# Kernel tuning notes

Measured on AMD Instinct MI355X. Metric: run time of the kernel, lower is better.

## Reference

```python
import jax, jax.numpy as jnp
import numpy as np

C = 256        # n_channels
CQK = 32       # n_query_key_channels (C // 8)
B = 16
HT, WT = 16, 16   # template feature map
HS, WS = 32, 32   # search-region feature map
K = 9             # 3x3 deformable kernel taps


def _conv1x1(x, w, b):
    # x [B,C,H,W], w [Co,Ci], b [Co]
    return jnp.einsum('bchw,oc->bohw', x, w) + b[None, :, None, None]


def _conv3x3(x, w, b):
    y = jax.lax.conv_general_dilated(x, w, (1, 1), 'SAME',
                                     dimension_numbers=('NCHW', 'OIHW', 'NCHW'))
    return y + b[None, :, None, None]


def _spatial_self_attn(x, qw, qb, kw, kb, vw, vb, weight=1.0):
    Bn, Cn, H, W = x.shape
    N = H * W
    q = _conv1x1(x, qw, qb).reshape(Bn, -1, N)   # [B,Cqk,N]
    k = _conv1x1(x, kw, kb).reshape(Bn, -1, N)
    v = _conv1x1(x, vw, vb).reshape(Bn, Cn, N)
    att = jnp.einsum('bcn,bcm->bnm', q, k)       # q^T k -> [B,N,N], no scaling (faithful)
    att = jax.nn.softmax(att, axis=0)            # softmax over BATCH dim, as in source
    out = weight * jnp.einsum('bcn,bnm->bcm', v, att)
    return out.reshape(x.shape)


def _channel_self_attn(x, weight=1.0):
    Bn, Cn, H, W = x.shape
    f = x.reshape(Bn, Cn, H * W)
    att = jnp.einsum('bcn,bdn->bcd', f, f)       # [B,C,C]
    att = jax.nn.softmax(att, axis=1)            # softmax over dim=1 (faithful)
    out = weight * jnp.einsum('bcd,bdn->bcn', att, f)
    return out.reshape(x.shape)


def _cross_attn(src, dst, weight=1.0):
    Bn, Cn = src.shape[:2]
    s = src.reshape(Bn, Cn, -1)
    d = dst.reshape(Bn, Cn, -1)
    att = jnp.einsum('bcn,bdn->bcd', s, s)       # CxC map from src only
    att = jax.nn.softmax(att, axis=1)
    out = weight * jnp.einsum('bcd,bdn->bcn', att, d)
    return out.reshape(dst.shape)


def _bilinear(img, y, x):
    # img [B,C,H,W]; y,x [B,K,H,W] float sampling coords -> [B,C,K,H,W], zeros outside
    Bn, Cn, H, W = img.shape
    y0 = jnp.floor(y)
    x0 = jnp.floor(x)
    wy1 = y - y0
    wx1 = x - x0

    def g(yi, xi):
        valid = ((yi >= 0) & (yi <= H - 1) & (xi >= 0) & (xi <= W - 1)).astype(img.dtype)
        yc = jnp.clip(yi, 0, H - 1).astype(jnp.int32)
        xc = jnp.clip(xi, 0, W - 1).astype(jnp.int32)
        bidx = jnp.arange(Bn)[:, None, None, None]
        v = img[bidx, :, yc, xc]                 # [B,K,H,W,C]
        return jnp.moveaxis(v, -1, 1) * valid[:, None]

    return (g(y0, x0) * ((1 - wy1) * (1 - wx1))[:, None]
            + g(y0, x0 + 1) * ((1 - wy1) * wx1)[:, None]
            + g(y0 + 1, x0) * (wy1 * (1 - wx1))[:, None]
            + g(y0 + 1, x0 + 1) * (wy1 * wx1)[:, None])


def _mod_deform_conv3x3(x, off_w, off_b, w, b):
    # mmcv ModulatedDeformConvPack: conv_offset -> chunk(o1,o2,mask); offset=cat(o1,o2); mask=sigmoid
    Bn, Cn, H, W = x.shape
    oo = _conv3x3(x, off_w, off_b)               # [B, 27, H, W]
    o1, o2, m = jnp.split(oo, 3, axis=1)
    offset = jnp.concatenate([o1, o2], axis=1)   # [B, 18, H, W]
    mask = jax.nn.sigmoid(m)                     # [B, 9, H, W]
    off_y = offset[:, 0::2]                      # channel 2k  -> y offset of tap k
    off_x = offset[:, 1::2]                      # channel 2k+1-> x offset of tap k
    ki, kj = jnp.meshgrid(jnp.arange(3), jnp.arange(3), indexing='ij')
    ki = ki.reshape(K).astype(jnp.float32)
    kj = kj.reshape(K).astype(jnp.float32)
    # stride 1, pad 1, dilation 1
    y = jnp.arange(H, dtype=jnp.float32)[None, None, :, None] - 1.0 + ki[None, :, None, None] + off_y
    xx = jnp.arange(W, dtype=jnp.float32)[None, None, None, :] - 1.0 + kj[None, :, None, None] + off_x
    sampled = _bilinear(x, y, xx) * mask[:, None]   # [B,C,K,H,W]
    out = jnp.einsum('bckhw,ock->bohw', sampled, w.reshape(w.shape[0], Cn, K))
    return out + b[None, :, None, None]


def _forward(template_features, sr_features,
             tq_w, tq_b, tk_w, tk_b, tv_w, tv_b,
             sq_w, sq_b, sk_w, sk_b, sv_w, sv_b,
             t_off_w, t_off_b, t_dcn_w, t_dcn_b,
             s_off_w, s_off_b, s_dcn_w, s_dcn_b):
    t, s = template_features, sr_features
    t_self = _spatial_self_attn(t, tq_w, tq_b, tk_w, tk_b, tv_w, tv_b) + _channel_self_attn(t)
    t_cross = _cross_attn(s, t)
    s_self = _spatial_self_attn(s, sq_w, sq_b, sk_w, sk_b, sv_w, sv_b) + _channel_self_attn(s)
    s_cross = _cross_attn(t, s)
    at = t + t_self + t_cross
    asr = s + s_self + s_cross
    out_t = _mod_deform_conv3x3(at, t_off_w, t_off_b, t_dcn_w, t_dcn_b)
    out_s = _mod_deform_conv3x3(asr, s_off_w, s_off_b, s_dcn_w, s_dcn_b)
    return (out_t, out_s)


def setup_inputs() -> dict:
    key = jax.random.key(0)
    ks = jax.random.split(key, 16)

    def rn(k, shape, s=1.0):
        return s * jax.random.normal(k, shape, dtype=jnp.float32)

    w1 = 1.0 / np.sqrt(C)          # 1x1 conv fan-in scale
    wd = 1.0 / np.sqrt(C * K)      # 3x3 conv fan-in scale
    inp = {
        'template_features': rn(ks[0], (B, C, HT, WT)),
        'sr_features': rn(ks[1], (B, C, HS, WS)),
        'tq_w': rn(ks[2], (CQK, C), w1), 'tq_b': jnp.zeros((CQK,), jnp.float32),
        'tk_w': rn(ks[3], (CQK, C), w1), 'tk_b': jnp.zeros((CQK,), jnp.float32),
        'tv_w': rn(ks[4], (C, C), w1), 'tv_b': jnp.zeros((C,), jnp.float32),
        'sq_w': rn(ks[5], (CQK, C), w1), 'sq_b': jnp.zeros((CQK,), jnp.float32),
        'sk_w': rn(ks[6], (CQK, C), w1), 'sk_b': jnp.zeros((CQK,), jnp.float32),
        'sv_w': rn(ks[7], (C, C), w1), 'sv_b': jnp.zeros((C,), jnp.float32),
        't_off_w': rn(ks[8], (3 * K, C, 3, 3), 0.01), 't_off_b': jnp.zeros((3 * K,), jnp.float32),
        't_dcn_w': rn(ks[9], (C, C, 3, 3), wd), 't_dcn_b': jnp.zeros((C,), jnp.float32),
        's_off_w': rn(ks[10], (3 * K, C, 3, 3), 0.01), 's_off_b': jnp.zeros((3 * K,), jnp.float32),
        's_dcn_w': rn(ks[11], (C, C, 3, 3), wd), 's_dcn_b': jnp.zeros((C,), jnp.float32),
    }
    return inp


def reference(template_features, sr_features,
              tq_w, tq_b, tk_w, tk_b, tv_w, tv_b,
              sq_w, sq_b, sk_w, sk_b, sv_w, sv_b,
              t_off_w, t_off_b, t_dcn_w, t_dcn_b,
              s_off_w, s_off_b, s_dcn_w, s_dcn_b):
    return _forward(template_features, sr_features,
                    tq_w, tq_b, tk_w, tk_b, tv_w, tv_b,
                    sq_w, sq_b, sk_w, sk_b, sv_w, sv_b,
                    t_off_w, t_off_b, t_dcn_w, t_dcn_b,
                    s_off_w, s_off_b, s_dcn_w, s_dcn_b)
```

## Files before the change

kernel.cpp:

```cpp
#include <hip/hip_runtime.h>
#include <hip/hip_bf16.h>

typedef __hip_bfloat16 bf16;
typedef __attribute__((ext_vector_type(8))) short short8;
typedef __attribute__((ext_vector_type(4))) short short4v;
typedef __attribute__((ext_vector_type(4))) float f32x4;

__device__ __forceinline__ short f2b(float v)
{
    union { bf16 b; short s; } u;
    u.b = __float2bfloat16(v);
    return u.s;
}
__device__ __forceinline__ float b2f(short s)
{
    union { short s; bf16 b; } u;
    u.s = s;
    return __bfloat162float(u.b);
}
__device__ __forceinline__ void splt(float v, short& hi, short& lo)
{
    hi = f2b(v);
    lo = f2b(v - b2f(hi));
}
__device__ __forceinline__ int bsw(int row, int g)
{
    return row * 40 + (((g + (row >> 3)) & 3) << 3);
}

__global__ void detect_k(const unsigned short* __restrict__ p, int* __restrict__ flag)
{
    __shared__ int cnt;
    if (threadIdx.x == 0) cnt = 0;
    __syncthreads();
    int bad = 0;
    for (int i = threadIdx.x; i < 4096; i += 256) {
        unsigned short u = p[2 * i];
        int e = (u >> 7) & 0xFF;
        if (e != 0 && (e < 100 || e > 140)) bad++;
    }
    atomicAdd(&cnt, bad);
    __syncthreads();
    if (threadIdx.x == 0) *flag = (cnt > 1024) ? 1 : 0;
}

#define NSEG 24
struct IArgs {
    const void* src[NSEG];
    float* dst[NSEG];
    long start[NSEG + 1];
};

__global__ void ingest_all_k(IArgs a, const int* __restrict__ flag)
{
    long i = (long)blockIdx.x * 256 + threadIdx.x;
    if (i >= a.start[NSEG]) return;
    int s = 0;
#pragma unroll
    for (int j = 1; j < NSEG; j++) s += (i >= a.start[j]) ? 1 : 0;
    long idx = i - a.start[s];
    float v;
    if (*flag) v = ((const float*)a.src[s])[idx];
    else       v = __bfloat162float(((const bf16*)a.src[s])[idx]);
    a.dst[s][idx] = v;
}

__global__ void fill_k(float* __restrict__ C, const float* __restrict__ bias,
                       long MN, int Nn, long total)
{
    long i = (long)blockIdx.x * 256 + threadIdx.x;
    if (i >= total) return;
    float v = 0.f;
    if (bias) {
        long r = i % MN;
        v = bias[(int)(r / Nn)];
    }
    C[i] = v;
}

__global__ void fillo_k(float* __restrict__ C1, const float* __restrict__ b1,
                        int N1, long tot1,
                        float* __restrict__ C2, const float* __restrict__ b2,
                        int N2, long tot2)
{
    long i = (long)blockIdx.x * 256 + threadIdx.x;
    if (i < tot1) {
        long r = i % ((long)27 * N1);
        C1[i] = b1[(int)(r / N1)];
    } else {
        i -= tot1;
        if (i < tot2) {
            long r = i % ((long)27 * N2);
            C2[i] = b2[(int)(r / N2)];
        }
    }
}

__global__ void tr2_k(const float* __restrict__ X1, float* __restrict__ T1, int N1,
                      const float* __restrict__ X2, float* __restrict__ T2, int N2)
{
    __shared__ float t[32][33];
    int bx = blockIdx.x;
    const float* X; float* T; int N, n0;
    int nb1 = N1 / 32;
    if (bx < nb1) { X = X1; T = T1; N = N1; n0 = bx * 32; }
    else          { X = X2; T = T2; N = N2; n0 = (bx - nb1) * 32; }
    int b = blockIdx.z, c0 = blockIdx.y * 32;
    const float* Xb = X + (long)b * 256 * N;
    float* Tb = T + (long)b * 256 * N;
    int tx = threadIdx.x, ty = threadIdx.y;
#pragma unroll
    for (int i = 0; i < 4; i++)
        t[ty + 8 * i][tx] = Xb[(long)(c0 + ty + 8 * i) * N + n0 + tx];
    __syncthreads();
#pragma unroll
    for (int i = 0; i < 4; i++)
        Tb[(long)(n0 + ty + 8 * i) * 256 + c0 + tx] = t[tx][ty + 8 * i];
}

template <bool TRA, int BMODE, bool ACCUM, bool BIAS, int PREC, int KSPLIT>
__launch_bounds__(256)
__global__ void mgemm(const float* __restrict__ A, int lda, int ksA, long sA,
                      const void* __restrict__ Bsrc, int ldb, long sB,
                      float* __restrict__ C, int ldc, long sC,
                      const float* __restrict__ bias,
                      int M, int N, int K, int H, int wsh)
{
    __shared__ short As[PREC * 2560];
    __shared__ short Bs[PREC * 2560];

    const int bz = blockIdx.z;
    const float* Ab = A + (long)bz * sA;
    float* Cb = C + (long)bz * sC;
    const int mt = blockIdx.y / KSPLIT, ch = blockIdx.y % KSPLIT;
    const int m0 = mt * 64, n0 = blockIdx.x * 64;
    const int kchunk = K / KSPLIT;
    const int kbeg = ch * kchunk, kend = kbeg + kchunk;
    const int tid = threadIdx.x;

    f32x4 acc[2][2];
#pragma unroll
    for (int i = 0; i < 2; i++)
#pragma unroll
        for (int j = 0; j < 2; j++) acc[i][j] = (f32x4){0.f, 0.f, 0.f, 0.f};

    const int lane = tid & 63, wv = tid >> 6;
    const int moff = (wv & 1) * 32, noff = (wv >> 1) * 32;
    const int lr = lane & 15, lq = lane >> 4;
    const int mm = tid >> 2, kk0 = (tid & 3) * 8;
    const int nn = tid & 63, kg = tid >> 6;

    for (int k0 = kbeg; k0 < kend; k0 += 32) {
        {
            float vv[8];
            if (m0 + mm < M) {
                if (!TRA) {
                    if (ksA == 1) {
                        const float4* s4 = (const float4*)(Ab + (long)(m0 + mm) * lda + k0 + kk0);
                        float4 v0 = s4[0], v1 = s4[1];
                        vv[0] = v0.x; vv[1] = v0.y; vv[2] = v0.z; vv[3] = v0.w;
                        vv[4] = v1.x; vv[5] = v1.y; vv[6] = v1.z; vv[7] = v1.w;
                    } else {
                        const float* s = Ab + (long)(m0 + mm) * lda + (long)(k0 + kk0) * ksA;
#pragma unroll
                        for (int j = 0; j < 8; j++) vv[j] = s[(long)j * ksA];
                    }
                } else {
#pragma unroll
                    for (int j = 0; j < 8; j++)
                        vv[j] = Ab[(long)(k0 + kk0 + j) * lda + m0 + mm];
                }
            } else {
#pragma unroll
                for (int j = 0; j < 8; j++) vv[j] = 0.f;
            }
            short8 hi, lo;
#pragma unroll
            for (int j = 0; j < 8; j++) { short h, l; splt(vv[j], h, l); hi[j] = h; lo[j] = l; }
            *(short8*)&As[mm * 40 + kk0] = hi;
            if (PREC == 2) *(short8*)&As[2560 + mm * 40 + kk0] = lo;
        }

        if (BMODE == 1) {
            const float4* s4 = (const float4*)((const float*)Bsrc + (long)bz * sB +
                                               (long)(n0 + mm) * ldb + k0 + kk0);
            float4 v0 = s4[0], v1 = s4[1];
            float vv[8] = {v0.x, v0.y, v0.z, v0.w, v1.x, v1.y, v1.z, v1.w};
            short8 hi, lo;
#pragma unroll
            for (int j = 0; j < 8; j++) { short h, l; splt(vv[j], h, l); hi[j] = h; lo[j] = l; }
            int o = bsw(mm, tid & 3);
            *(short8*)&Bs[o] = hi;
            if (PREC == 2) *(short8*)&Bs[2560 + o] = lo;
        } else {
            float vv[8];
            if (BMODE == 0) {
#pragma unroll
                for (int j = 0; j < 8; j++)
                    vv[j] = ((const float*)Bsrc)[(long)bz * sB + (long)(k0 + kg * 8 + j) * ldb + n0 + nn];
            } else {
                int W = 1 << wsh;
                int n = n0 + nn;
                int hbase = n >> wsh, wbase = n & (W - 1);
#pragma unroll
                for (int j = 0; j < 8; j++) {
                    int kc = k0 + kg * 8 + j;
                    int c = kc / 9, tap = kc - 9 * c;
                    int h = hbase + tap / 3 - 1, w = wbase + tap % 3 - 1;
                    vv[j] = (h >= 0 && h < H && w >= 0 && w < W)
                          ? ((const float*)Bsrc)[(long)bz * sB + (long)c * ldb + (h << wsh) + w]
                          : 0.f;
                }
            }
            short8 hi, lo;
#pragma unroll
            for (int j = 0; j < 8; j++) { short h, l; splt(vv[j], h, l); hi[j] = h; lo[j] = l; }
            int o = bsw(nn, kg);
            *(short8*)&Bs[o] = hi;
            if (PREC == 2) *(short8*)&Bs[2560 + o] = lo;
        }
        __syncthreads();

        int rb0 = noff + lr, rb1 = noff + 16 + lr;
        short8 a0h = *(short8*)&As[(moff + lr) * 40 + lq * 8];
        short8 a1h = *(short8*)&As[(moff + 16 + lr) * 40 + lq * 8];
        short8 b0h = *(short8*)&Bs[bsw(rb0, lq)];
        short8 b1h = *(short8*)&Bs[bsw(rb1, lq)];
        acc[0][0] = __builtin_amdgcn_mfma_f32_16x16x32_bf16(a0h, b0h, acc[0][0], 0, 0, 0);
        acc[0][1] = __builtin_amdgcn_mfma_f32_16x16x32_bf16(a0h, b1h, acc[0][1], 0, 0, 0);
        acc[1][0] = __builtin_amdgcn_mfma_f32_16x16x32_bf16(a1h, b0h, acc[1][0], 0, 0, 0);
        acc[1][1] = __builtin_amdgcn_mfma_f32_16x16x32_bf16(a1h, b1h, acc[1][1], 0, 0, 0);
        if (PREC == 2) {
            short8 a0l = *(short8*)&As[2560 + (moff + lr) * 40 + lq * 8];
            short8 a1l = *(short8*)&As[2560 + (moff + 16 + lr) * 40 + lq * 8];
            short8 b0l = *(short8*)&Bs[2560 + bsw(rb0, lq)];
            short8 b1l = *(short8*)&Bs[2560 + bsw(rb1, lq)];
            acc[0][0] = __builtin_amdgcn_mfma_f32_16x16x32_bf16(a0h, b0l, acc[0][0], 0, 0, 0);
            acc[0][1] = __builtin_amdgcn_mfma_f32_16x16x32_bf16(a0h, b1l, acc[0][1], 0, 0, 0);
            acc[1][0] = __builtin_amdgcn_mfma_f32_16x16x32_bf16(a1h, b0l, acc[1][0], 0, 0, 0);
            acc[1][1] = __builtin_amdgcn_mfma_f32_16x16x32_bf16(a1h, b1l, acc[1][1], 0, 0, 0);
            acc[0][0] = __builtin_amdgcn_mfma_f32_16x16x32_bf16(a0l, b0h, acc[0][0], 0, 0, 0);
            acc[0][1] = __builtin_amdgcn_mfma_f32_16x16x32_bf16(a0l, b1h, acc[0][1], 0, 0, 0);
            acc[1][0] = __builtin_amdgcn_mfma_f32_16x16x32_bf16(a1l, b0h, acc[1][0], 0, 0, 0);
            acc[1][1] = __builtin_amdgcn_mfma_f32_16x16x32_bf16(a1l, b1h, acc[1][1], 0, 0, 0);
        }
        __syncthreads();
    }

#pragma unroll
    for (int mi = 0; mi < 2; mi++)
#pragma unroll
        for (int ni = 0; ni < 2; ni++) {
            int col = n0 + noff + ni * 16 + lr;
#pragma unroll
            for (int r = 0; r < 4; r++) {
                int row = m0 + moff + mi * 16 + lq * 4 + r;
                if (row < M) {
                    long o = (long)row * ldc + col;
                    float v = acc[mi][ni][r];
                    if (KSPLIT > 1) {
                        atomicAdd(&Cb[o], v);
                    } else {
                        if (BIAS) v += bias[row];
                        if (ACCUM) v += Cb[o];
                        Cb[o] = v;
                    }
                }
            }
        }
}

__global__ void dcnw2_k(const float* __restrict__ OOt, float4* __restrict__ Twt,
                        int4* __restrict__ Tat,
                        const float* __restrict__ OOs, float4* __restrict__ Tws,
                        int4* __restrict__ Tas)
{
    long idx = (long)blockIdx.x * 256 + threadIdx.x;
    const long n1 = 16L * 9 * 256;
    const long n2 = 16L * 9 * 1024;
    const float* OO; float4* Tw; int4* Ta; int N, H, W;
    if (idx < n1) { OO = OOt; Tw = Twt; Ta = Tat; N = 256; H = 16; W = 16; }
    else {
        idx -= n1;
        if (idx >= n2) return;
        OO = OOs; Tw = Tws; Ta = Tas; N = 1024; H = 32; W = 32;
    }
    int b = (int)(idx / (9 * N));
    int r = (int)(idx % (9 * N));
    int tap = r / N, p = r % N;
    int h = p / W, w = p % W;
    const float* oob = OO + (long)b * 27 * N;
    float oy = oob[(2 * tap) * N + p];
    float ox = oob[(2 * tap + 1) * N + p];
    float mz = oob[(18 + tap) * N + p];
    float mask = 1.f / (1.f + expf(-mz));
    float y = (float)(h - 1 + tap / 3) + oy;
    float x = (float)(w - 1 + tap % 3) + ox;
    float y0 = floorf(y), x0 = floorf(x);
    float wy = y - y0, wx = x - x0;
    float ys[2] = {y0, y0 + 1.f};
    float xs[2] = {x0, x0 + 1.f};
    float wys[2] = {1.f - wy, wy};
    float wxs[2] = {1.f - wx, wx};
    float wv[4]; int av[4];
#pragma unroll
    for (int iy = 0; iy < 2; iy++)
#pragma unroll
        for (int ix = 0; ix < 2; ix++) {
            float yy = ys[iy], xx = xs[ix];
            bool valid = (yy >= 0.f) && (yy <= (float)(H - 1)) &&
                         (xx >= 0.f) && (xx <= (float)(W - 1));
            wv[iy * 2 + ix] = valid ? wys[iy] * wxs[ix] * mask : 0.f;
            int yc = (int)fminf(fmaxf(yy, 0.f), (float)(H - 1));
            int xc = (int)fminf(fmaxf(xx, 0.f), (float)(W - 1));
            av[iy * 2 + ix] = yc * W + xc;
        }
    long o = (long)(b * 9 + tap) * N + p;
    Tw[o] = (float4){wv[0], wv[1], wv[2], wv[3]};
    Ta[o] = (int4){av[0], av[1], av[2], av[3]};
}

__global__ void wre5_k(const float* __restrict__ Wt, short* __restrict__ Wht,
                       const float* __restrict__ Ws, short* __restrict__ Whs)
{
    long idx = (long)blockIdx.x * 256 + threadIdx.x;
    const long half = 2304L * 256;
    const float* W; short* Wh;
    if (idx < half) { W = Wt; Wh = Wht; }
    else            { W = Ws; Wh = Whs; idx -= half; }
    int o = (int)(idx / 2304);
    int k = (int)(idx % 2304);
    int tap = k >> 8, c = k & 255;
    Wh[(long)o * 2304 + tap * 256 + c] = f2b(W[((long)o * 256 + c) * 9 + tap]);
}

__global__ void samp2_k(const float4* __restrict__ Twt, const int4* __restrict__ Tat,
                        const float* __restrict__ XTt, short* __restrict__ Sit,
                        const float4* __restrict__ Tws, const int4* __restrict__ Tas,
                        const float* __restrict__ XTs, short* __restrict__ Sis)
{
    int bx = blockIdx.x;
    const float4* Tw; const int4* Ta; const float* XT; short* Si;
    int N, NRND, nblk;
    if (bx < 4) { Tw = Twt; Ta = Tat; XT = XTt; Si = Sit; N = 256;  NRND = 256;  nblk = bx; }
    else        { Tw = Tws; Ta = Tas; XT = XTs; Si = Sis; N = 1024; NRND = 1024; nblk = bx - 4; }

    int tid = threadIdx.x;
    int g = tid >> 2, cc2 = tid & 3;
    int tap = blockIdx.y, b = blockIdx.z;
    int n = nblk * 64 + g;
    long ti = ((long)(b * 9 + tap)) * N + n;
    float4 w4 = Tw[ti];
    int4 a4 = Ta[ti];
    const float* Xb = XT + (long)b * 256 * N;
    const float4* r0 = (const float4*)(Xb + (long)a4.x * 256);
    const float4* r1 = (const float4*)(Xb + (long)a4.y * 256);
    const float4* r2 = (const float4*)(Xb + (long)a4.z * 256);
    const float4* r3 = (const float4*)(Xb + (long)a4.w * 256);
    long so = ((long)b * NRND + n) * 2304 + tap * 256;
    short4v out[16];
#pragma unroll
    for (int q = 0; q < 16; q++) {
        int i = q * 4 + cc2;
        float4 p = r0[i], qv = r1[i], s = r2[i], t = r3[i];
        out[q][0] = f2b(w4.x * p.x + w4.y * qv.x + w4.z * s.x + w4.w * t.x);
        out[q][1] = f2b(w4.x * p.y + w4.y * qv.y + w4.z * s.y + w4.w * t.y);
        out[q][2] = f2b(w4.x * p.z + w4.y * qv.z + w4.z * s.z + w4.w * t.z);
        out[q][3] = f2b(w4.x * p.w + w4.y * qv.w + w4.z * s.w + w4.w * t.w);
    }
#pragma unroll
    for (int q = 0; q < 16; q++)
        *(short4v*)&Si[so + q * 16 + cc2 * 4] = out[q];
}

__launch_bounds__(256, 4)
__global__ void dcn9_k(const short* __restrict__ Wh_s, const short* __restrict__ Si_s,
                       const short* __restrict__ Wh_t, const short* __restrict__ Si_t,
                       const float* __restrict__ bias_s, const float* __restrict__ bias_t,
                       float* __restrict__ Cs, float* __restrict__ Ct)
{
    __shared__ float red[8192];

    int bid = blockIdx.x;
    const short* Wh; const short* Si; const float* bias; float* Cb;
    int N, mt, nt;
    if (bid < 1024) {
        int bz = bid >> 6, t = bid & 63;
        mt = t >> 4; nt = t & 15;
        Wh = Wh_s; Si = Si_s + (long)bz * 1024 * 2304;
        bias = bias_s; Cb = Cs + (long)bz * 256 * 1024; N = 1024;
    } else {
        int r = bid - 1024;
        int bz = r >> 4, t = r & 15;
        mt = t >> 2; nt = t & 3;
        Wh = Wh_t; Si = Si_t + (long)bz * 256 * 2304;
        bias = bias_t; Cb = Ct + (long)bz * 256 * 256; N = 256;
    }
    const int m0 = mt * 64, n0 = nt * 64;

    const int tid = threadIdx.x;
    const int lane = tid & 63, wv = tid >> 6;
    const int lr = lane & 15, lq = lane >> 4;

    int aoff[4], boff[4];
#pragma unroll
    for (int mi = 0; mi < 4; mi++)
        aoff[mi] = (m0 + mi * 16 + lr) * 2304 + lq * 8;
#pragma unroll
    for (int ni = 0; ni < 4; ni++)
        boff[ni] = (n0 + ni * 16 + lr) * 2304 + lq * 8;

    f32x4 acc[4][4];
#pragma unroll
    for (int i = 0; i < 4; i++)
#pragma unroll
        for (int j = 0; j < 4; j++) acc[i][j] = (f32x4){0.f, 0.f, 0.f, 0.f};

    const int kbeg = wv * 18;
#pragma unroll 2
    for (int kt = kbeg; kt < kbeg + 18; kt++) {
        int koff = (kt >> 3) * 256 + (kt & 7) * 32;
        short8 ah[4], bh[4];
#pragma unroll
        for (int ni = 0; ni < 4; ni++)
            bh[ni] = *(const short8*)&Si[boff[ni] + koff];
#pragma unroll
        for (int mi = 0; mi < 4; mi++)
            ah[mi] = *(const short8*)&Wh[aoff[mi] + koff];
#pragma unroll
        for (int mi = 0; mi < 4; mi++)
#pragma unroll
            for (int ni = 0; ni < 4; ni++)
                acc[mi][ni] = __builtin_amdgcn_mfma_f32_16x16x32_bf16(ah[mi], bh[ni], acc[mi][ni], 0, 0, 0);
    }

    if (wv == 1 || wv == 3) {
        float* rp = &red[(wv == 1 ? 0 : 4096) + lane];
#pragma unroll
        for (int mi = 0; mi < 4; mi++)
#pragma unroll
            for (int ni = 0; ni < 4; ni++)
#pragma unroll
                for (int r2 = 0; r2 < 4; r2++)
                    rp[(mi * 16 + ni * 4 + r2) << 6] = acc[mi][ni][r2];
    }
    __syncthreads();
    if (wv == 0) {
        const float* rp = &red[lane];
#pragma unroll
        for (int mi = 0; mi < 4; mi++)
#pragma unroll
            for (int ni = 0; ni < 4; ni++)
#pragma unroll
                for (int r2 = 0; r2 < 4; r2++)
                    acc[mi][ni][r2] += rp[(mi * 16 + ni * 4 + r2) << 6];
    } else if (wv == 2) {
        float* rp = &red[4096 + lane];
#pragma unroll
        for (int mi = 0; mi < 4; mi++)
#pragma unroll
            for (int ni = 0; ni < 4; ni++)
#pragma unroll
                for (int r2 = 0; r2 < 4; r2++) {
                    int o = (mi * 16 + ni * 4 + r2) << 6;
                    float v = acc[mi][ni][r2] + rp[o];
                    rp[o] = v;
                }
    }
    __syncthreads();
    if (wv == 0) {
        const float* rp = &red[4096 + lane];
#pragma unroll
        for (int mi = 0; mi < 4; mi++)
#pragma unroll
            for (int ni = 0; ni < 4; ni++) {
                int col = n0 + ni * 16 + lr;
#pragma unroll
                for (int r2 = 0; r2 < 4; r2++) {
                    int row = m0 + mi * 16 + lq * 4 + r2;
                    float v = acc[mi][ni][r2] + rp[(mi * 16 + ni * 4 + r2) << 6];
                    Cb[(long)row * N + col] = v + bias[row];
                }
            }
    }
}

__global__ void softmax_b_k(float* __restrict__ att, long NN)
{
    long idx = (long)blockIdx.x * 256 + threadIdx.x;
    if (idx >= NN) return;
    float r[16];
    float mx = -1e30f;
#pragma unroll
    for (int b = 0; b < 16; b++) {
        r[b] = att[(long)b * NN + idx];
        mx = fmaxf(mx, r[b]);
    }
    float s = 0.f;
#pragma unroll
    for (int b = 0; b < 16; b++) { r[b] = expf(r[b] - mx); s += r[b]; }
    float inv = 1.f / s;
#pragma unroll
    for (int b = 0; b < 16; b++) att[(long)b * NN + idx] = r[b] * inv;
}

__global__ void gram_sm_k(const float* __restrict__ gt, const float* __restrict__ gs,
                          float* __restrict__ Mo)
{
    int b = blockIdx.x;
    int d = blockIdx.y * 64 + threadIdx.x;
    const float* gtb = gt + (long)b * 65536;
    const float* gsb = gs + (long)b * 65536;
    float* mb = Mo + (long)b * 65536;
    float mt = -1e30f, ms = -1e30f;
    for (int c = 0; c < 256; c++) {
        mt = fmaxf(mt, gtb[c * 256 + d]);
        ms = fmaxf(ms, gsb[c * 256 + d]);
    }
    float st = 0.f, ss = 0.f;
    for (int c = 0; c < 256; c++) {
        st += expf(gtb[c * 256 + d] - mt);
        ss += expf(gsb[c * 256 + d] - ms);
    }
    float it = 1.f / st, is = 1.f / ss;
    for (int c = 0; c < 256; c++)
        mb[c * 256 + d] = expf(gtb[c * 256 + d] - mt) * it +
                          expf(gsb[c * 256 + d] - ms) * is;
}

__global__ void cast_out_k(const float* __restrict__ t, const float* __restrict__ s,
                           void* __restrict__ out, long nt, long ntot,
                           const int* __restrict__ flag)
{
    long idx = (long)blockIdx.x * 256 + threadIdx.x;
    if (idx >= ntot) return;
    float v = (idx < nt) ? t[idx] : s[idx - nt];
    if (*flag) ((float*)out)[idx] = v;
    else       ((bf16*)out)[idx] = __float2bfloat16(v);
}

extern "C" void kernel_launch(void* const* d_in, const int* in_sizes, int n_in,
                              void* d_out, int out_size, void* d_ws, size_t ws_size,
                              hipStream_t stream)
{
    const int B = 16, C = 256;
    const int Nt = 256, Ns = 1024;
    const long sXt = (long)C * Nt, sXs = (long)C * Ns;
    dim3 blk(256);

    float* ws = (float*)d_ws;
    int* flag = (int*)d_ws;
    long off = 16;
    auto alloc = [&](long n) { float* p = ws + off; off += n; return p; };

    float* xt32     = alloc((long)B * C * Nt);
    float* xs32     = alloc((long)B * C * Ns);
    float* Wf       = alloc(1470464);
    float* q_t      = alloc((long)B * 32 * Nt);
    float* k_t      = alloc((long)B * 32 * Nt);
    float* v_t      = alloc((long)B * C * Nt);
    float* q_s      = alloc((long)B * 32 * Ns);
    float* k_s      = alloc((long)B * 32 * Ns);
    float* v_s      = alloc((long)B * C * Ns);
    float* gram_t   = alloc((long)B * C * C);
    float* gram_s   = alloc((long)B * C * C);
    float* Mc       = alloc((long)B * C * C);
    float* att_t    = alloc((long)B * Nt * Nt);
    float* att_slab = alloc((long)B * Ns * 256);
    float* at       = alloc((long)B * C * Nt);
    float* asr      = alloc((long)B * C * Ns);
    float* oo_t     = alloc((long)B * 27 * Nt);
    float* oo_s     = alloc((long)B * 27 * Ns);
    float* Si_f     = alloc(18874368);
    short* Si = (short*)Si_f;
    float* att_full = Si_f;

    float* out_t_f32 = gram_t;
    float* out_s_f32 = xs32;
    float* xtT       = att_t;
    float* xsT       = att_slab;
    float* atT       = att_t;
    float* asrT      = att_slab;
    short* Si_t = (short*)at;
    short* Wi_t = (short*)v_s;
    short* Wi_s = (short*)v_s + 589824;
    float* tb   = v_s + 1179648;
    float4* Tw_t = (float4*)tb;
    int4*   Ta_t = (int4*)(tb + 147456);
    float4* Tw_s = (float4*)(tb + 2 * 147456);
    int4*   Ta_s = (int4*)(tb + 2 * 147456 + 589824);

    detect_k<<<dim3(1), blk, 0, stream>>>((const unsigned short*)d_in[0], flag);
    long woff[22];
    {
        long acc = 0;
        for (int i = 2; i < 22; i++) { woff[i] = acc; acc += (in_sizes[i] + 7) & ~7L; }
    }
    IArgs ia;
    long tot = 0;
    auto seg = [&](int s, const void* src, float* dst, long n) {
        ia.src[s] = src; ia.dst[s] = dst; ia.start[s] = tot; tot += n;
    };
    seg(0, d_in[0], xt32, (long)B * C * Nt);
    seg(1, d_in[0], at,   (long)B * C * Nt);
    seg(2, d_in[1], xs32, (long)B * C * Ns);
    seg(3, d_in[1], asr,  (long)B * C * Ns);
    for (int i = 2; i < 22; i++) seg(2 + i, d_in[i], Wf + woff[i], in_sizes[i]);
    ia.start[NSEG] = tot;
    ingest_all_k<<<dim3((unsigned)((tot + 255) / 256)), blk, 0, stream>>>(ia, flag);

    const float *tq_w = Wf + woff[2],  *tq_b = Wf + woff[3];
    const float *tk_w = Wf + woff[4],  *tk_b = Wf + woff[5];
    const float *tv_w = Wf + woff[6],  *tv_b = Wf + woff[7];
    const float *sq_w = Wf + woff[8],  *sq_b = Wf + woff[9];
    const float *sk_w = Wf + woff[10], *sk_b = Wf + woff[11];
    const float *sv_w = Wf + woff[12], *sv_b = Wf + woff[13];
    const float *t_off_w = Wf + woff[14], *t_off_b = Wf + woff[15];
    const float *t_dcn_w = Wf + woff[16], *t_dcn_b = Wf + woff[17];
    const float *s_off_w = Wf + woff[18], *s_off_b = Wf + woff[19];
    const float *s_dcn_w = Wf + woff[20], *s_dcn_b = Wf + woff[21];

    tr2_k<<<dim3((Nt + Ns) / 32, 8, B), dim3(32, 8), 0, stream>>>(
        xt32, xtT, Nt, xs32, xsT, Ns);
    fill_k<<<dim3((2 * B * C * C) / 256), blk, 0, stream>>>(gram_t, nullptr, 1, 1, 2L * B * C * C);
    fillo_k<<<dim3((unsigned)((B * 27L * (Nt + Ns) + 255) / 256)), blk, 0, stream>>>(
        oo_t, t_off_b, Nt, (long)B * 27 * Nt,
        oo_s, s_off_b, Ns, (long)B * 27 * Ns);

    mgemm<false, 1, false, true, 2, 1><<<dim3(Nt / 64, 1, B), blk, 0, stream>>>(
        tq_w, 256, 1, 0, xtT, 256, sXt, q_t, Nt, (long)32 * Nt, tq_b, 32, Nt, 256, 0, 0);
    mgemm<false, 1, false, true, 2, 1><<<dim3(Nt / 64, 1, B), blk, 0, stream>>>(
        tk_w, 256, 1, 0, xtT, 256, sXt, k_t, Nt, (long)32 * Nt, tk_b, 32, Nt, 256, 0, 0);
    mgemm<false, 1, false, true, 2, 1><<<dim3(Nt / 64, 4, B), blk, 0, stream>>>(
        tv_w, 256, 1, 0, xtT, 256, sXt, v_t, Nt, sXt, tv_b, 256, Nt, 256, 0, 0);
    mgemm<false, 1, false, true, 2, 1><<<dim3(Ns / 64, 1, B), blk, 0, stream>>>(
        sq_w, 256, 1, 0, xsT, 256, sXs, q_s, Ns, (long)32 * Ns, sq_b, 32, Ns, 256, 0, 0);
    mgemm<false, 1, false, true, 2, 1><<<dim3(Ns / 64, 1, B), blk, 0, stream>>>(
        sk_w, 256, 1, 0, xsT, 256, sXs, k_s, Ns, (long)32 * Ns, sk_b, 32, Ns, 256, 0, 0);
    mgemm<false, 1, false, true, 2, 1><<<dim3(Ns / 64, 4, B), blk, 0, stream>>>(
        sv_w, 256, 1, 0, xsT, 256, sXs, v_s, Ns, sXs, sv_b, 256, Ns, 256, 0, 0);

    mgemm<false, 1, false, false, 1, 4><<<dim3(4, 16, B), blk, 0, stream>>>(
        xt32, Nt, 1, sXt, xt32, Nt, sXt, gram_t, 256, (long)C * C, nullptr, 256, 256, Nt, 0, 0);
    mgemm<false, 1, false, false, 1, 4><<<dim3(4, 16, B), blk, 0, stream>>>(
        xs32, Ns, 1, sXs, xs32, Ns, sXs, gram_s, 256, (long)C * C, nullptr, 256, 256, Ns, 0, 0);

    gram_sm_k<<<dim3(B, 4), dim3(64), 0, stream>>>(gram_t, gram_s, Mc);

    mgemm<false, 1, true, false, 2, 2><<<dim3(Nt / 64, 8, B), blk, 0, stream>>>(
        Mc, 256, 1, (long)C * C, xtT, 256, sXt, at, Nt, sXt, nullptr, 256, Nt, 256, 0, 0);
    mgemm<false, 1, true, false, 2, 1><<<dim3(Ns / 64, 4, B), blk, 0, stream>>>(
        Mc, 256, 1, (long)C * C, xsT, 256, sXs, asr, Ns, sXs, nullptr, 256, Ns, 256, 0, 0);

    mgemm<true, 0, false, false, 2, 1><<<dim3(4, 4, B), blk, 0, stream>>>(
        k_t, Nt, 1, (long)32 * Nt, q_t, Nt, (long)32 * Nt, att_t, Nt, (long)Nt * Nt,
        nullptr, Nt, Nt, 32, 0, 0);
    softmax_b_k<<<dim3((Nt * Nt) / 256), blk, 0, stream>>>(att_t, (long)Nt * Nt);
    mgemm<false, 1, true, false, 2, 2><<<dim3(Nt / 64, 8, B), blk, 0, stream>>>(
        v_t, Nt, 1, sXt, att_t, Nt, (long)Nt * Nt, at, Nt, sXt, nullptr, 256, Nt, Nt, 0, 0);

    mgemm<true, 0, false, false, 2, 1><<<dim3(Ns / 64, Ns / 64, B), blk, 0, stream>>>(
        k_s, Ns, 1, (long)32 * Ns, q_s, Ns, (long)32 * Ns,
        att_full, Ns, (long)Ns * Ns, nullptr, Ns, Ns, 32, 0, 0);
    softmax_b_k<<<dim3((unsigned)(((long)Ns * Ns) / 256)), blk, 0, stream>>>(
        att_full, (long)Ns * Ns);
    mgemm<false, 1, true, false, 2, 1><<<dim3(Ns / 64, 4, B), blk, 0, stream>>>(
        v_s, Ns, 1, sXs, att_full, Ns, (long)Ns * Ns,
        asr, Ns, sXs, nullptr, 256, Ns, Ns, 0, 0);

    mgemm<false, 3, false, false, 2, 4><<<dim3(Nt / 64, 4, B), blk, 0, stream>>>(
        t_off_w, 2304, 1, 0, at, Nt, sXt, oo_t, Nt, (long)27 * Nt,
        nullptr, 27, Nt, 2304, 16, 4);
    mgemm<false, 3, false, false, 2, 4><<<dim3(Ns / 64, 4, B), blk, 0, stream>>>(
        s_off_w, 2304, 1, 0, asr, Ns, sXs, oo_s, Ns, (long)27 * Ns,
        nullptr, 27, Ns, 2304, 32, 5);

    wre5_k<<<dim3(4608), blk, 0, stream>>>(t_dcn_w, Wi_t, s_dcn_w, Wi_s);
    dcnw2_k<<<dim3((unsigned)((16L * 9 * (Nt + Ns)) / 256)), blk, 0, stream>>>(
        oo_t, Tw_t, Ta_t, oo_s, Tw_s, Ta_s);
    tr2_k<<<dim3((Nt + Ns) / 32, 8, B), dim3(32, 8), 0, stream>>>(
        at, atT, Nt, asr, asrT, Ns);

    samp2_k<<<dim3(20, 9, B), blk, 0, stream>>>(
        Tw_t, Ta_t, atT, Si_t, Tw_s, Ta_s, asrT, Si);
    dcn9_k<<<dim3(1280), blk, 0, stream>>>(Wi_s, Si, Wi_t, Si_t,
                                           s_dcn_b, t_dcn_b, out_s_f32, out_t_f32);

    long nt = (long)B * C * Nt;
    long ntot = nt + (long)B * C * Ns;
    cast_out_k<<<dim3((unsigned)((ntot + 255) / 256)), blk, 0, stream>>>(
        out_t_f32, out_s_f32, d_out, nt, ntot, flag);
}
```

Baseline: 720.6 us.

## Fuse Q/K/V projections into one GEMM and parallelize gram softmax

The ingest step now writes the separate query, key and value weights and biases into one contiguous 320-row weight matrix per branch. This replaces six small projection GEMM launches with two larger ones. Downstream attention GEMMs read q, k and v as slices of the fused output using a 320-row batch stride. The gram column-softmax kernel is also rewritten from 64 blocks of 64 serial-loop threads into 256 blocks of 256 threads, with shared-memory max and sum reductions, to raise parallelism. The risk is that the aliased workspace buffers (Wi, tb placed in qkv_s) must still fit and not overlap live data.

Measured after the change: 638.8 us. 11.3% less time.

```diff
diff --git a/kernel.cpp b/kernel.cpp
--- a/kernel.cpp
+++ b/kernel.cpp
@@ -504,26 +504,62 @@
     for (int b = 0; b < 16; b++) att[(long)b * NN + idx] = r[b] * inv;
 }
 
-__global__ void gram_sm_k(const float* __restrict__ gt, const float* __restrict__ gs,
-                          float* __restrict__ Mo)
-{
+__global__ void gram_sm2_k(const float* __restrict__ gt, const float* __restrict__ gs,
+                           float* __restrict__ Mo)
+{
+    __shared__ float red[2][17][16];
     int b = blockIdx.x;
-    int d = blockIdx.y * 64 + threadIdx.x;
+    int td = threadIdx.x & 15;
+    int tc = threadIdx.x >> 4;
+    int d = blockIdx.y * 16 + td;
     const float* gtb = gt + (long)b * 65536;
     const float* gsb = gs + (long)b * 65536;
     float* mb = Mo + (long)b * 65536;
+
     float mt = -1e30f, ms = -1e30f;
-    for (int c = 0; c < 256; c++) {
+    for (int c = tc * 16; c < tc * 16 + 16; c++) {
         mt = fmaxf(mt, gtb[c * 256 + d]);
         ms = fmaxf(ms, gsb[c * 256 + d]);
     }
+    red[0][tc][td] = mt;
+    red[1][tc][td] = ms;
+    __syncthreads();
+    if (tc == 0) {
+        float a = -1e30f, bb = -1e30f;
+        for (int i = 0; i < 16; i++) {
+            a = fmaxf(a, red[0][i][td]);
+            bb = fmaxf(bb, red[1][i][td]);
+        }
+        red[0][16][td] = a;
+        red[1][16][td] = bb;
+    }
+    __syncthreads();
+    mt = red[0][16][td];
+    ms = red[1][16][td];
+    __syncthreads();
+
     float st = 0.f, ss = 0.f;
-    for (int c = 0; c < 256; c++) {
+    for (int c = tc * 16; c < tc * 16 + 16; c++) {
         st += expf(gtb[c * 256 + d] - mt);
         ss += expf(gsb[c * 256 + d] - ms);
     }
-    float it = 1.f / st, is = 1.f / ss;
-    for (int c = 0; c < 256; c++)
+    red[0][tc][td] = st;
+    red[1][tc][td] = ss;
+    __syncthreads();
+    if (tc == 0) {
+        float a = 0.f, bb = 0.f;
+        for (int i = 0; i < 16; i++) {
+            a += red[0][i][td];
+            bb += red[1][i][td];
+        }
+        red[0][16][td] = a;
+        red[1][16][td] = bb;
+    }
+    __syncthreads();
+    float it = 1.f / red[0][16][td];
+    float is = 1.f / red[1][16][td];
+
+    for (int c = tc * 16; c < tc * 16 + 16; c++)
         mb[c * 256 + d] = expf(gtb[c * 256 + d] - mt) * it +
                           expf(gsb[c * 256 + d] - ms) * is;
 }
@@ -556,12 +592,12 @@
     float* xt32     = alloc((long)B * C * Nt);
     float* xs32     = alloc((long)B * C * Ns);
     float* Wf       = alloc(1470464);
-    float* q_t      = alloc((long)B * 32 * Nt);
-    float* k_t      = alloc((long)B * 32 * Nt);
-    float* v_t      = alloc((long)B * C * Nt);
-    float* q_s      = alloc((long)B * 32 * Ns);
-    float* k_s      = alloc((long)B * 32 * Ns);
-    float* v_s      = alloc((long)B * C * Ns);
+    float* qkv_t    = alloc((long)B * 320 * Nt);
+    float* qkv_s    = alloc((long)B * 320 * Ns);
+    float* Wqkv_t   = alloc(81920);
+    float* bqkv_t   = alloc(320);
+    float* Wqkv_s   = alloc(81920);
+    float* bqkv_s   = alloc(320);
     float* gram_t   = alloc((long)B * C * C);
     float* gram_s   = alloc((long)B * C * C);
     float* Mc       = alloc((long)B * C * C);
@@ -582,9 +618,9 @@
     float* atT       = att_t;
     float* asrT      = att_slab;
     short* Si_t = (short*)at;
-    short* Wi_t = (short*)v_s;
-    short* Wi_s = (short*)v_s + 589824;
-    float* tb   = v_s + 1179648;
+    short* Wi_t = (short*)qkv_s;
+    short* Wi_s = (short*)qkv_s + 589824;
+    float* tb   = qkv_s + 1179648;
     float4* Tw_t = (float4*)tb;
     int4*   Ta_t = (int4*)(tb + 147456);
     float4* Tw_s = (float4*)(tb + 2 * 147456);
@@ -596,6 +632,14 @@
         long acc = 0;
         for (int i = 2; i < 22; i++) { woff[i] = acc; acc += (in_sizes[i] + 7) & ~7L; }
     }
+    float* wdst[22];
+    for (int i = 2; i < 22; i++) wdst[i] = Wf + woff[i];
+    wdst[2]  = Wqkv_t;          wdst[3]  = bqkv_t;
+    wdst[4]  = Wqkv_t + 8192;   wdst[5]  = bqkv_t + 32;
+    wdst[6]  = Wqkv_t + 16384;  wdst[7]  = bqkv_t + 64;
+    wdst[8]  = Wqkv_s;          wdst[9]  = bqkv_s;
+    wdst[10] = Wqkv_s + 8192;   wdst[11] = bqkv_s + 32;
+    wdst[12] = Wqkv_s + 16384;  wdst[13] = bqkv_s + 64;
     IArgs ia;
     long tot = 0;
     auto seg = [&](int s, const void* src, float* dst, long n) {
@@ -605,16 +649,10 @@
     seg(1, d_in[0], at,   (long)B * C * Nt);
     seg(2, d_in[1], xs32, (long)B * C * Ns);
     seg(3, d_in[1], asr,  (long)B * C * Ns);
-    for (int i = 2; i < 22; i++) seg(2 + i, d_in[i], Wf + woff[i], in_sizes[i]);
+    for (int i = 2; i < 22; i++) seg(2 + i, d_in[i], wdst[i], in_sizes[i]);
     ia.start[NSEG] = tot;
     ingest_all_k<<<dim3((unsigned)((tot + 255) / 256)), blk, 0, stream>>>(ia, flag);
 
-    const float *tq_w = Wf + woff[2],  *tq_b = Wf + woff[3];
-    const float *tk_w = Wf + woff[4],  *tk_b = Wf + woff[5];
-    const float *tv_w = Wf + woff[6],  *tv_b = Wf + woff[7];
-    const float *sq_w = Wf + woff[8],  *sq_b = Wf + woff[9];
-    const float *sk_w = Wf + woff[10], *sk_b = Wf + woff[11];
-    const float *sv_w = Wf + woff[12], *sv_b = Wf + woff[13];
     const float *t_off_w = Wf + woff[14], *t_off_b = Wf + woff[15];
     const float *t_dcn_w = Wf + woff[16], *t_dcn_b = Wf + woff[17];
     const float *s_off_w = Wf + woff[18], *s_off_b = Wf + woff[19];
@@ -627,25 +665,17 @@
         oo_t, t_off_b, Nt, (long)B * 27 * Nt,
         oo_s, s_off_b, Ns, (long)B * 27 * Ns);
 
-    mgemm<false, 1, false, true, 2, 1><<<dim3(Nt / 64, 1, B), blk, 0, stream>>>(
-        tq_w, 256, 1, 0, xtT, 256, sXt, q_t, Nt, (long)32 * Nt, tq_b, 32, Nt, 256, 0, 0);
-    mgemm<false, 1, false, true, 2, 1><<<dim3(Nt / 64, 1, B), blk, 0, stream>>>(
-        tk_w, 256, 1, 0, xtT, 256, sXt, k_t, Nt, (long)32 * Nt, tk_b, 32, Nt, 256, 0, 0);
-    mgemm<false, 1, false, true, 2, 1><<<dim3(Nt / 64, 4, B), blk, 0, stream>>>(
-        tv_w, 256, 1, 0, xtT, 256, sXt, v_t, Nt, sXt, tv_b, 256, Nt, 256, 0, 0);
-    mgemm<false, 1, false, true, 2, 1><<<dim3(Ns / 64, 1, B), blk, 0, stream>>>(
-        sq_w, 256, 1, 0, xsT, 256, sXs, q_s, Ns, (long)32 * Ns, sq_b, 32, Ns, 256, 0, 0);
-    mgemm<false, 1, false, true, 2, 1><<<dim3(Ns / 64, 1, B), blk, 0, stream>>>(
-        sk_w, 256, 1, 0, xsT, 256, sXs, k_s, Ns, (long)32 * Ns, sk_b, 32, Ns, 256, 0, 0);
-    mgemm<false, 1, false, true, 2, 1><<<dim3(Ns / 64, 4, B), blk, 0, stream>>>(
-        sv_w, 256, 1, 0, xsT, 256, sXs, v_s, Ns, sXs, sv_b, 256, Ns, 256, 0, 0);
+    mgemm<false, 1, false, true, 2, 1><<<dim3(Nt / 64, 5, B), blk, 0, stream>>>(
+        Wqkv_t, 256, 1, 0, xtT, 256, sXt, qkv_t, Nt, (long)320 * Nt, bqkv_t, 320, Nt, 256, 0, 0);
+    mgemm<false, 1, false, true, 2, 1><<<dim3(Ns / 64, 5, B), blk, 0, stream>>>(
+        Wqkv_s, 256, 1, 0, xsT, 256, sXs, qkv_s, Ns, (long)320 * Ns, bqkv_s, 320, Ns, 256, 0, 0);
 
     mgemm<false, 1, false, false, 1, 4><<<dim3(4, 16, B), blk, 0, stream>>>(
         xt32, Nt, 1, sXt, xt32, Nt, sXt, gram_t, 256, (long)C * C, nullptr, 256, 256, Nt, 0, 0);
     mgemm<false, 1, false, false, 1, 4><<<dim3(4, 16, B), blk, 0, stream>>>(
         xs32, Ns, 1, sXs, xs32, Ns, sXs, gram_s, 256, (long)C * C, nullptr, 256, 256, Ns, 0, 0);
 
-    gram_sm_k<<<dim3(B, 4), dim3(64), 0, stream>>>(gram_t, gram_s, Mc);
+    gram_sm2_k<<<dim3(B, 16), blk, 0, stream>>>(gram_t, gram_s, Mc);
 
     mgemm<false, 1, true, false, 2, 2><<<dim3(Nt / 64, 8, B), blk, 0, stream>>>(
         Mc, 256, 1, (long)C * C, xtT, 256, sXt, at, Nt, sXt, nullptr, 256, Nt, 256, 0, 0);
@@ -653,19 +683,20 @@
         Mc, 256, 1, (long)C * C, xsT, 256, sXs, asr, Ns, sXs, nullptr, 256, Ns, 256, 0, 0);
 
     mgemm<true, 0, false, false, 2, 1><<<dim3(4, 4, B), blk, 0, stream>>>(
-        k_t, Nt, 1, (long)32 * Nt, q_t, Nt, (long)32 * Nt, att_t, Nt, (long)Nt * Nt,
-        nullptr, Nt, Nt, 32, 0, 0);
+        qkv_t + 32 * Nt, Nt, 1, (long)320 * Nt, qkv_t, Nt, (long)320 * Nt,
+        att_t, Nt, (long)Nt * Nt, nullptr, Nt, Nt, 32, 0, 0);
     softmax_b_k<<<dim3((Nt * Nt) / 256), blk, 0, stream>>>(att_t, (long)Nt * Nt);
     mgemm<false, 1, true, false, 2, 2><<<dim3(Nt / 64, 8, B), blk, 0, stream>>>(
-        v_t, Nt, 1, sXt, att_t, Nt, (long)Nt * Nt, at, Nt, sXt, nullptr, 256, Nt, Nt, 0, 0);
+        qkv_t + 64 * Nt, Nt, 1, (long)320 * Nt, att_t, Nt, (long)Nt * Nt,
+        at, Nt, sXt, nullptr, 256, Nt, Nt, 0, 0);
 
     mgemm<true, 0, false, false, 2, 1><<<dim3(Ns / 64, Ns / 64, B), blk, 0, stream>>>(
-        k_s, Ns, 1, (long)32 * Ns, q_s, Ns, (long)32 * Ns,
+        qkv_s + 32 * Ns, Ns, 1, (long)320 * Ns, qkv_s, Ns, (long)320 * Ns,
         att_full, Ns, (long)Ns * Ns, nullptr, Ns, Ns, 32, 0, 0);
     softmax_b_k<<<dim3((unsigned)(((long)Ns * Ns) / 256)), blk, 0, stream>>>(
         att_full, (long)Ns * Ns);
     mgemm<false, 1, true, false, 2, 1><<<dim3(Ns / 64, 4, B), blk, 0, stream>>>(
-        v_s, Ns, 1, sXs, att_full, Ns, (long)Ns * Ns,
+        qkv_s + 64 * Ns, Ns, 1, (long)320 * Ns, att_full, Ns, (long)Ns * Ns,
         asr, Ns, sXs, nullptr, 256, Ns, Ns, 0, 0);
 
     mgemm<false, 3, false, false, 2, 4><<<dim3(Nt / 64, 4, B), blk, 0, stream>>>(
```
